# Optimization experiments

Hardware: AMD Instinct MI355X
Metric: run time of the kernel (lower is better)

## Reference

```python
import jax, jax.numpy as jnp
import numpy as np

GROUPS = 32
EPS = 1e-6


def group_norm(x, gamma, beta):
    b, c, h, w = x.shape
    xg = x.reshape(b, GROUPS, c // GROUPS, h, w)
    mu = xg.mean(axis=(2, 3, 4), keepdims=True)
    var = xg.var(axis=(2, 3, 4), keepdims=True)
    xn = ((xg - mu) * jax.lax.rsqrt(var + EPS)).reshape(b, c, h, w)
    return xn * gamma[None, :, None, None] + beta[None, :, None, None]


def conv1x1(x, w, b):
    # x: (b,c_in,h,w), w: (c_out,c_in), b: (c_out,)
    return jnp.einsum('oc,bchw->bohw', w, x) + b[None, :, None, None]


def setup_inputs() -> dict:
    key = jax.random.key(0)
    ks = jax.random.split(key, 10)
    c = 512
    scale = 1.0 / np.sqrt(c)
    inp = jax.random.normal(ks[0], (16, c, 32, 32), dtype=jnp.float32)
    return {
        'inp': inp,
        'gamma': jnp.ones((c,), jnp.float32),
        'beta': jnp.zeros((c,), jnp.float32),
        'Wq': jax.random.normal(ks[1], (c, c), jnp.float32) * scale,
        'bq': jnp.zeros((c,), jnp.float32),
        'Wk': jax.random.normal(ks[2], (c, c), jnp.float32) * scale,
        'bk': jnp.zeros((c,), jnp.float32),
        'Wv': jax.random.normal(ks[3], (c, c), jnp.float32) * scale,
        'bv': jnp.zeros((c,), jnp.float32),
        'Wo': jax.random.normal(ks[4], (c, c), jnp.float32) * scale,
        'bo': jnp.zeros((c,), jnp.float32),
    }


def reference(inp, gamma, beta, Wq, bq, Wk, bk, Wv, bv, Wo, bo):
    b, c, h, w = inp.shape
    x = group_norm(inp, gamma, beta)
    Q = conv1x1(x, Wq, bq).reshape(b, c, h * w)  # (b,c,n)
    K = conv1x1(x, Wk, bk).reshape(b, c, h * w)  # (b,c,m)
    V = conv1x1(x, Wv, bv).reshape(b, c, h * w)  # (b,c,m)
    # attn[b,n,m] = sum_c Q[b,c,n] * K[b,c,m], scaled then softmax over m
    attn = jnp.einsum('bcn,bcm->bnm', Q, K) / jnp.sqrt(jnp.float32(c))
    attn = jax.nn.softmax(attn, axis=2)
    # A[b,c,n] = sum_m V[b,c,m] * attn[b,n,m]  (== bmm(V, attn^T))
    A = jnp.einsum('bcm,bnm->bcn', V, attn).reshape(b, c, h, w)
    A = conv1x1(A, Wo, bo)
    return inp + A
```

## Files before the change

### kernel.cpp

```cpp
#include <hip/hip_runtime.h>

typedef unsigned short UST;
typedef __attribute__((ext_vector_type(8))) short bf16x8;
typedef __attribute__((ext_vector_type(8))) unsigned short us8;
typedef __attribute__((ext_vector_type(4))) float f32x4;

__device__ __forceinline__ UST f2bf(float f) {
  union { float f; unsigned int u; } x; x.f = f;
  unsigned int r = x.u + 0x7fffu + ((x.u >> 16) & 1u);
  return (UST)(r >> 16);
}
__device__ __forceinline__ float bf2f(UST h) {
  union { unsigned int u; float f; } x; x.u = ((unsigned int)h) << 16;
  return x.f;
}

typedef const __attribute__((address_space(1))) unsigned int* gptr32;
typedef __attribute__((address_space(3))) unsigned int* lptr32;

__device__ __forceinline__ void load16(const void* g, void* l) {
  __builtin_amdgcn_global_load_lds((gptr32)(unsigned long long)g,
                                   (lptr32)(unsigned int)(unsigned long long)l,
                                   16, 0, 0);
}

__global__ __launch_bounds__(256) void conv_w(
    const float4* __restrict__ wq, const float4* __restrict__ wk,
    const float4* __restrict__ wv, const float4* __restrict__ wo,
    ushort4* __restrict__ oqkv, ushort4* __restrict__ owo,
    const float4* __restrict__ bq4, const float4* __restrict__ bk4,
    const float4* __restrict__ bv4, float4* __restrict__ bqkv4) {
  int i = blockIdx.x * 256 + threadIdx.x;
  float4 v;
  v = wq[i]; oqkv[i]          = make_ushort4(f2bf(v.x), f2bf(v.y), f2bf(v.z), f2bf(v.w));
  v = wk[i]; oqkv[i + 65536]  = make_ushort4(f2bf(v.x), f2bf(v.y), f2bf(v.z), f2bf(v.w));
  v = wv[i]; oqkv[i + 131072] = make_ushort4(f2bf(v.x), f2bf(v.y), f2bf(v.z), f2bf(v.w));
  v = wo[i]; owo[i]           = make_ushort4(f2bf(v.x), f2bf(v.y), f2bf(v.z), f2bf(v.w));
  if (blockIdx.x < 2) {
    int t = blockIdx.x * 256 + threadIdx.x;
    if (t < 384) bqkv4[t] = (t < 128) ? bq4[t] : (t < 256 ? bk4[t - 128] : bv4[t - 256]);
  }
}

__global__ __launch_bounds__(256) void gn_fused(
    const float* __restrict__ inp, const float* __restrict__ gamma,
    const float* __restrict__ beta, UST* __restrict__ Xnt) {
  const int g = blockIdx.x & 31, b = blockIdx.x >> 5;
  const int tid = threadIdx.x;
  const float* base = inp + ((size_t)b * 32 + g) * 16384;
  const float4* p4 = (const float4*)base;
  float s = 0.f, ss = 0.f;
#pragma unroll
  for (int i = 0; i < 16; i++) {
    float4 t = p4[tid + i * 256];
    s += t.x + t.y + t.z + t.w;
    ss += t.x * t.x + t.y * t.y + t.z * t.z + t.w * t.w;
  }
  for (int o = 32; o >= 1; o >>= 1) { s += __shfl_xor(s, o); ss += __shfl_xor(ss, o); }
  __shared__ float red[8];
  __shared__ float mu_s, rstd_s;
  const int w = tid >> 6;
  if ((tid & 63) == 0) { red[w * 2] = s; red[w * 2 + 1] = ss; }
  __syncthreads();
  if (tid == 0) {
    float S1 = red[0] + red[2] + red[4] + red[6];
    float S2 = red[1] + red[3] + red[5] + red[7];
    float mu = S1 * (1.f / 16384.f);
    float var = S2 * (1.f / 16384.f) - mu * mu;
    mu_s = mu; rstd_s = rsqrtf(var + 1e-6f);
  }
  __syncthreads();
  const float mu = mu_s, rstd = rstd_s;
#pragma unroll
  for (int cc = 0; cc < 2; cc++) {
    const int ccg = g * 2 + cc;
    float sc[8], sh[8];
#pragma unroll
    for (int j = 0; j < 8; j++) {
      int ch = ccg * 8 + j;
      sc[j] = gamma[ch] * rstd;
      sh[j] = beta[ch] - mu * sc[j];
    }
#pragma unroll
    for (int i = 0; i < 4; i++) {
      const int n = tid + i * 256;
      us8 v;
#pragma unroll
      for (int j = 0; j < 8; j++) {
        float x = inp[((size_t)b * 512 + ccg * 8 + j) * 1024 + n];
        v[j] = f2bf(x * sc[j] + sh[j]);
      }
      *(us8*)(Xnt + (size_t)b * 524288 + (size_t)ccg * 8192 + (size_t)n * 8) = v;
    }
  }
}

__global__ __launch_bounds__(256) void softmax_k(const UST* __restrict__ S,
                                                 UST* __restrict__ P) {
  const int w = threadIdx.x >> 6, lane = threadIdx.x & 63;
  const size_t row = (size_t)blockIdx.x * 4 + w;
  const us8* Sr = (const us8*)(S + row * 1024);
  us8 a = Sr[lane], b = Sr[64 + lane];
  float v[16];
#pragma unroll
  for (int j = 0; j < 8; j++) { v[j] = bf2f(a[j]); v[8 + j] = bf2f(b[j]); }
  float m = v[0];
#pragma unroll
  for (int i = 1; i < 16; i++) m = fmaxf(m, v[i]);
#pragma unroll
  for (int o = 32; o >= 1; o >>= 1) m = fmaxf(m, __shfl_xor(m, o));
  float s = 0.f;
#pragma unroll
  for (int i = 0; i < 16; i++) { v[i] = __expf(v[i] - m); s += v[i]; }
#pragma unroll
  for (int o = 32; o >= 1; o >>= 1) s += __shfl_xor(s, o);
  const float rs = 1.f / s;
  us8* Pr = (us8*)(P + row * 1024);
  us8 oa, ob;
#pragma unroll
  for (int j = 0; j < 8; j++) { oa[j] = f2bf(v[j] * rs); ob[j] = f2bf(v[8 + j] * rs); }
  Pr[lane] = oa; Pr[64 + lane] = ob;
}

template <int EPI>
__global__ __launch_bounds__(256, 2) void gemm_bt(
    const UST* __restrict__ A, const UST* __restrict__ B, void* __restrict__ C,
    const float* __restrict__ bias, const float* __restrict__ extra, float scale,
    int K, int ldc,
    int rsA, int csA, int ssA, int rsB, int csB, int ssB,
    long zA, long zB, long zC) {
  __shared__ __align__(16) UST buf[17408];
  UST* lA = buf;
  UST* lB = buf + 4096;

  const int tid = threadIdx.x;
  const int z = blockIdx.z;
  const int m0 = blockIdx.y * 128;
  const int n0 = blockIdx.x * 128;
  const UST* Ab = A + (long)z * zA;
  const UST* Bb = B + (long)z * zB;

  const int w = tid >> 6, lane = tid & 63;
  const int quad = lane >> 4, l16 = lane & 15;
  const int wm = w >> 1, wn = w & 1;

  f32x4 acc[4][4];
#pragma unroll
  for (int i = 0; i < 4; i++)
#pragma unroll
    for (int j = 0; j < 4; j++) acc[i][j] = f32x4{0.f, 0.f, 0.f, 0.f};

  const int rowa = tid >> 2;
  const int kchunk = tid & 3;
  const UST* gA = Ab + (size_t)(m0 + rowa) * rsA + (size_t)kchunk * csA;
  const UST* gB = Bb + (size_t)(n0 + rowa) * rsB + (size_t)kchunk * csB;
  char* lAw = (char*)lA + (w << 10);
  char* lBw = (char*)lB + (w << 10);

  for (int k0 = 0; k0 < K; k0 += 32) {
    __syncthreads();
    load16(gA, lAw);
    load16(gA + (size_t)64 * rsA, lAw + 4096);
    load16(gB, lBw);
    load16(gB + (size_t)64 * rsB, lBw + 4096);
    gA += ssA; gB += ssB;
    __syncthreads();
    bf16x8 af[4], bfr[4];
#pragma unroll
    for (int i = 0; i < 4; i++)
      af[i] = *(const bf16x8*)(lA + (wm * 64 + i * 16 + l16) * 32 + quad * 8);
#pragma unroll
    for (int j = 0; j < 4; j++)
      bfr[j] = *(const bf16x8*)(lB + (wn * 64 + j * 16 + l16) * 32 + quad * 8);
#pragma unroll
    for (int i = 0; i < 4; i++)
#pragma unroll
      for (int j = 0; j < 4; j++)
        acc[i][j] = __builtin_amdgcn_mfma_f32_16x16x32_bf16(af[i], bfr[j], acc[i][j], 0, 0, 0);
  }

  __syncthreads();

  if constexpr (EPI == 4) {
    float* fbuf = (float*)buf;
    float* Cb = (float*)C + (long)z * zC;
    const float* Eb = extra + (long)z * zC;
#pragma unroll
    for (int h = 0; h < 2; h++) {
      if (wm == h) {
#pragma unroll
        for (int i = 0; i < 4; i++)
#pragma unroll
          for (int j = 0; j < 4; j++)
#pragma unroll
            for (int r = 0; r < 4; r++)
              fbuf[(i * 16 + quad * 4 + r) * 132 + wn * 64 + j * 16 + l16] = acc[i][j][r];
      }
      __syncthreads();
#pragma unroll
      for (int it = 0; it < 8; it++) {
        int q = tid + it * 256;
        int row = q >> 5, colc = q & 31;
        int gr = m0 + h * 64 + row;
        size_t off = (size_t)gr * ldc + n0 + colc * 4;
        float4 v = *(float4*)&fbuf[row * 132 + colc * 4];
        float4 e = *(const float4*)&Eb[off];
        float bb = bias[gr];
        v.x += bb + e.x; v.y += bb + e.y; v.z += bb + e.z; v.w += bb + e.w;
        *(float4*)&Cb[off] = v;
      }
      __syncthreads();
    }
  } else {
    const bool vreg = (EPI == 6) && (n0 >= 1024);
#pragma unroll
    for (int i = 0; i < 4; i++)
#pragma unroll
      for (int j = 0; j < 4; j++) {
        float bc = 0.f;
        if constexpr (EPI == 6) bc = bias[n0 + wn * 64 + j * 16 + l16];
#pragma unroll
        for (int r = 0; r < 4; r++) {
          float v = acc[i][j][r] + bc;
          if constexpr (EPI == 5) v *= scale;
          const int lr = wm * 64 + i * 16 + quad * 4 + r;
          const int lc = wn * 64 + j * 16 + l16;
          if (!vreg) buf[lr * 136 + lc] = f2bf(v);
          else       buf[lc * 136 + lr] = f2bf(v);
        }
      }
    __syncthreads();
    if (!vreg) {
      UST* Cb = (UST*)C + (long)z * zC;
#pragma unroll
      for (int it = 0; it < 8; it++) {
        int q = tid + it * 256;
        int row = q >> 4, colc = q & 15;
        us8 v = *(us8*)&buf[row * 136 + colc * 8];
        *(us8*)&Cb[(size_t)(m0 + row) * ldc + n0 + colc * 8] = v;
      }
    } else {
      UST* Vb = (UST*)extra + (long)z * 524288;
#pragma unroll
      for (int it = 0; it < 8; it++) {
        int q = tid + it * 256;
        int c = q >> 4, mc = q & 15;
        us8 v = *(us8*)&buf[c * 136 + mc * 8];
        *(us8*)&Vb[(size_t)(n0 - 1024 + c) * 1024 + m0 + mc * 8] = v;
      }
    }
  }
}

extern "C" void kernel_launch(void* const* d_in, const int* in_sizes, int n_in,
                              void* d_out, int out_size, void* d_ws, size_t ws_size,
                              hipStream_t stream) {
  const float* inp   = (const float*)d_in[0];
  const float* gamma = (const float*)d_in[1];
  const float* beta  = (const float*)d_in[2];
  const float* Wq    = (const float*)d_in[3];
  const float* bq    = (const float*)d_in[4];
  const float* Wk    = (const float*)d_in[5];
  const float* bk    = (const float*)d_in[6];
  const float* Wv    = (const float*)d_in[7];
  const float* bv    = (const float*)d_in[8];
  const float* Wo    = (const float*)d_in[9];
  const float* bo    = (const float*)d_in[10];
  float* out = (float*)d_out;
  char* ws = (char*)d_ws;

  UST*   Xnt   = (UST*)(ws);
  UST*   QKt   = (UST*)(ws + ((size_t)16 << 20));
  UST*   V     = (UST*)(ws + ((size_t)48 << 20));
  UST*   S     = (UST*)(ws + ((size_t)64 << 20));
  float* bqkv  = (float*)(ws + ((size_t)96 << 20));
  UST*   Wqkvb = (UST*)(ws + ((size_t)96 << 20) + 8192);
  UST*   Wob   = Wqkvb + 786432;
  UST*   P     = QKt;
  UST*   At    = Xnt;

  conv_w<<<256, 256, 0, stream>>>(
      (const float4*)Wq, (const float4*)Wk, (const float4*)Wv, (const float4*)Wo,
      (ushort4*)Wqkvb, (ushort4*)Wob,
      (const float4*)bq, (const float4*)bk, (const float4*)bv, (float4*)bqkv);
  gn_fused<<<512, 256, 0, stream>>>(inp, gamma, beta, Xnt);

  gemm_bt<6><<<dim3(12, 8, 16), 256, 0, stream>>>(
      Xnt, Wqkvb, QKt, bqkv, (const float*)V, 1.f,
      512, 1024, 8, 8192, 32768, 512, 8, 32, 524288, 0, 1048576);
  gemm_bt<5><<<dim3(8, 8, 16), 256, 0, stream>>>(
      QKt, QKt + 512, S, nullptr, nullptr, 0.04419417382415922f,
      512, 1024, 1024, 8, 32, 1024, 8, 32, 1048576, 1048576, 1048576);
  softmax_k<<<4096, 256, 0, stream>>>(S, P);
  gemm_bt<3><<<dim3(4, 8, 16), 256, 0, stream>>>(
      P, V, At, nullptr, nullptr, 1.f,
      1024, 512, 1024, 8, 32, 1024, 8, 32, 1048576, 524288, 524288);
  gemm_bt<4><<<dim3(8, 4, 16), 256, 0, stream>>>(
      Wob, At, out, bo, inp, 1.f,
      512, 1024, 512, 8, 32, 512, 8, 32, 0, 524288, 524288);
}
```

Before: 244.9 us.

## Register-prefetch GEMM tiles with padded LDS and shrink epilogue staging buffer

```diff
diff --git a/kernel.cpp b/kernel.cpp
--- a/kernel.cpp
+++ b/kernel.cpp
@@ -15,13 +15,11 @@
   return x.f;
 }
 
-typedef const __attribute__((address_space(1))) unsigned int* gptr32;
-typedef __attribute__((address_space(3))) unsigned int* lptr32;
-
-__device__ __forceinline__ void load16(const void* g, void* l) {
-  __builtin_amdgcn_global_load_lds((gptr32)(unsigned long long)g,
-                                   (lptr32)(unsigned int)(unsigned long long)l,
-                                   16, 0, 0);
+__device__ __forceinline__ void sync_lds() {
+  asm volatile("s_waitcnt lgkmcnt(0)\n\ts_barrier" ::: "memory");
+}
+__device__ __forceinline__ void barrier_nowait() {
+  asm volatile("s_barrier" ::: "memory");
 }
 
 __global__ __launch_bounds__(256) void conv_w(
@@ -129,9 +127,9 @@
     int K, int ldc,
     int rsA, int csA, int ssA, int rsB, int csB, int ssB,
     long zA, long zB, long zC) {
-  __shared__ __align__(16) UST buf[17408];
+  __shared__ __align__(16) UST buf[10240];
   UST* lA = buf;
-  UST* lB = buf + 4096;
+  UST* lB = buf + 5120;
 
   const int tid = threadIdx.x;
   const int z = blockIdx.z;
@@ -154,54 +152,66 @@
   const int kchunk = tid & 3;
   const UST* gA = Ab + (size_t)(m0 + rowa) * rsA + (size_t)kchunk * csA;
   const UST* gB = Bb + (size_t)(n0 + rowa) * rsB + (size_t)kchunk * csB;
-  char* lAw = (char*)lA + (w << 10);
-  char* lBw = (char*)lB + (w << 10);
-
-  for (int k0 = 0; k0 < K; k0 += 32) {
-    __syncthreads();
-    load16(gA, lAw);
-    load16(gA + (size_t)64 * rsA, lAw + 4096);
-    load16(gB, lBw);
-    load16(gB + (size_t)64 * rsB, lBw + 4096);
-    gA += ssA; gB += ssB;
-    __syncthreads();
+  const size_t a64 = (size_t)64 * rsA, b64 = (size_t)64 * rsB;
+  UST* wA = lA + rowa * 40 + kchunk * 8;
+  UST* wB = lB + rowa * 40 + kchunk * 8;
+
+  us8 pa0 = *(const us8*)gA, pa1 = *(const us8*)(gA + a64);
+  us8 pb0 = *(const us8*)gB, pb1 = *(const us8*)(gB + b64);
+
+  const int nk = K >> 5;
+  for (int k = 0; k < nk; ++k) {
+    us8 na0, na1, nb0, nb1;
+    if (k + 1 < nk) {
+      gA += ssA; gB += ssB;
+      na0 = *(const us8*)gA; na1 = *(const us8*)(gA + a64);
+      nb0 = *(const us8*)gB; nb1 = *(const us8*)(gB + b64);
+    }
+    if (k) barrier_nowait();
+    *(us8*)wA = pa0; *(us8*)(wA + 2560) = pa1;
+    *(us8*)wB = pb0; *(us8*)(wB + 2560) = pb1;
+    sync_lds();
     bf16x8 af[4], bfr[4];
 #pragma unroll
     for (int i = 0; i < 4; i++)
-      af[i] = *(const bf16x8*)(lA + (wm * 64 + i * 16 + l16) * 32 + quad * 8);
+      af[i] = *(const bf16x8*)(lA + (wm * 64 + i * 16 + l16) * 40 + quad * 8);
 #pragma unroll
     for (int j = 0; j < 4; j++)
-      bfr[j] = *(const bf16x8*)(lB + (wn * 64 + j * 16 + l16) * 32 + quad * 8);
+      bfr[j] = *(const bf16x8*)(lB + (wn * 64 + j * 16 + l16) * 40 + quad * 8);
 #pragma unroll
     for (int i = 0; i < 4; i++)
 #pragma unroll
       for (int j = 0; j < 4; j++)
         acc[i][j] = __builtin_amdgcn_mfma_f32_16x16x32_bf16(af[i], bfr[j], acc[i][j], 0, 0, 0);
-  }
-
-  __syncthreads();
+    pa0 = na0; pa1 = na1; pb0 = nb0; pb1 = nb1;
+  }
+
+  barrier_nowait();
 
   if constexpr (EPI == 4) {
     float* fbuf = (float*)buf;
     float* Cb = (float*)C + (long)z * zC;
     const float* Eb = extra + (long)z * zC;
 #pragma unroll
-    for (int h = 0; h < 2; h++) {
-      if (wm == h) {
-#pragma unroll
-        for (int i = 0; i < 4; i++)
+    for (int p = 0; p < 4; ++p) {
+      if (p) barrier_nowait();
+      if (wm == (p >> 1)) {
+#pragma unroll
+        for (int ii = 0; ii < 2; ii++) {
+          const int i = (p & 1) * 2 + ii;
 #pragma unroll
           for (int j = 0; j < 4; j++)
 #pragma unroll
             for (int r = 0; r < 4; r++)
-              fbuf[(i * 16 + quad * 4 + r) * 132 + wn * 64 + j * 16 + l16] = acc[i][j][r];
-      }
-      __syncthreads();
-#pragma unroll
-      for (int it = 0; it < 8; it++) {
+              fbuf[(ii * 16 + quad * 4 + r) * 132 + wn * 64 + j * 16 + l16] = acc[i][j][r];
+        }
+      }
+      sync_lds();
+#pragma unroll
+      for (int it = 0; it < 4; ++it) {
         int q = tid + it * 256;
         int row = q >> 5, colc = q & 31;
-        int gr = m0 + h * 64 + row;
+        int gr = m0 + p * 32 + row;
         size_t off = (size_t)gr * ldc + n0 + colc * 4;
         float4 v = *(float4*)&fbuf[row * 132 + colc * 4];
         float4 e = *(const float4*)&Eb[off];
@@ -209,44 +219,64 @@
         v.x += bb + e.x; v.y += bb + e.y; v.z += bb + e.z; v.w += bb + e.w;
         *(float4*)&Cb[off] = v;
       }
-      __syncthreads();
     }
   } else {
     const bool vreg = (EPI == 6) && (n0 >= 1024);
-#pragma unroll
-    for (int i = 0; i < 4; i++)
-#pragma unroll
-      for (int j = 0; j < 4; j++) {
-        float bc = 0.f;
-        if constexpr (EPI == 6) bc = bias[n0 + wn * 64 + j * 16 + l16];
-#pragma unroll
-        for (int r = 0; r < 4; r++) {
-          float v = acc[i][j][r] + bc;
-          if constexpr (EPI == 5) v *= scale;
-          const int lr = wm * 64 + i * 16 + quad * 4 + r;
-          const int lc = wn * 64 + j * 16 + l16;
-          if (!vreg) buf[lr * 136 + lc] = f2bf(v);
-          else       buf[lc * 136 + lr] = f2bf(v);
-        }
-      }
-    __syncthreads();
     if (!vreg) {
       UST* Cb = (UST*)C + (long)z * zC;
 #pragma unroll
-      for (int it = 0; it < 8; it++) {
-        int q = tid + it * 256;
-        int row = q >> 4, colc = q & 15;
-        us8 v = *(us8*)&buf[row * 136 + colc * 8];
-        *(us8*)&Cb[(size_t)(m0 + row) * ldc + n0 + colc * 8] = v;
+      for (int h = 0; h < 2; ++h) {
+        if (h) barrier_nowait();
+        if (wm == h) {
+#pragma unroll
+          for (int i = 0; i < 4; i++)
+#pragma unroll
+            for (int j = 0; j < 4; j++) {
+              float bc = 0.f;
+              if constexpr (EPI == 6) bc = bias[n0 + wn * 64 + j * 16 + l16];
+#pragma unroll
+              for (int r = 0; r < 4; r++) {
+                float v = acc[i][j][r] + bc;
+                if constexpr (EPI == 5) v *= scale;
+                buf[(i * 16 + quad * 4 + r) * 136 + wn * 64 + j * 16 + l16] = f2bf(v);
+              }
+            }
+        }
+        sync_lds();
+#pragma unroll
+        for (int it = 0; it < 4; ++it) {
+          int q = tid + it * 256;
+          int row = q >> 4, colc = q & 15;
+          us8 v = *(us8*)&buf[row * 136 + colc * 8];
+          *(us8*)&Cb[(size_t)(m0 + h * 64 + row) * ldc + n0 + colc * 8] = v;
+        }
       }
     } else {
       UST* Vb = (UST*)extra + (long)z * 524288;
 #pragma unroll
-      for (int it = 0; it < 8; it++) {
-        int q = tid + it * 256;
-        int c = q >> 4, mc = q & 15;
-        us8 v = *(us8*)&buf[c * 136 + mc * 8];
-        *(us8*)&Vb[(size_t)(n0 - 1024 + c) * 1024 + m0 + mc * 8] = v;
+      for (int h = 0; h < 2; ++h) {
+        if (h) barrier_nowait();
+        if (wn == h) {
+#pragma unroll
+          for (int i = 0; i < 4; i++)
+#pragma unroll
+            for (int j = 0; j < 4; j++) {
+              const float bc = bias[n0 + wn * 64 + j * 16 + l16];
+#pragma unroll
+              for (int r = 0; r < 4; r++) {
+                float v = acc[i][j][r] + bc;
+                buf[(j * 16 + l16) * 136 + wm * 64 + i * 16 + quad * 4 + r] = f2bf(v);
+              }
+            }
+        }
+        sync_lds();
+#pragma unroll
+        for (int it = 0; it < 4; ++it) {
+          int q = tid + it * 256;
+          int c = q >> 4, mc = q & 15;
+          us8 v = *(us8*)&buf[c * 136 + mc * 8];
+          *(us8*)&Vb[(size_t)(n0 - 1024 + h * 64 + c) * 1024 + m0 + mc * 8] = v;
+        }
       }
     }
   }
```

New measurement: 238.5 us. 1.03x faster.
